# Optimization experiments

Hardware: AMD Instinct MI355X
Metric: run time of the kernel (lower is better)

Reference implementation:

```python
import jax, jax.numpy as jnp
import numpy as np

B, S, D, F, E, SH, K = 2, 2048, 2048, 1024, 16, 2, 2


def setup_inputs() -> dict:
    key = jax.random.key(0)
    ks = jax.random.split(key, 8)
    std = 0.02
    mk = lambda k, sh: (jax.random.normal(k, sh, jnp.float32) * std)
    return {
        "x": jax.random.normal(ks[0], (B, S, D), jnp.float32),
        "wa": mk(ks[1], (D, E)),                      # router, no bias
        "rg": mk(ks[2], (E, D, F)), "rgb": jnp.zeros((E, F), jnp.float32),
        "rw1": mk(ks[3], (E, D, F)), "rb1": jnp.zeros((E, F), jnp.float32),
        "rw2": mk(ks[4], (E, F, D)), "rb2": jnp.zeros((E, D), jnp.float32),
        "sg": mk(ks[5], (SH, D, F)), "sgb": jnp.zeros((SH, F), jnp.float32),
        "sw1": mk(ks[6], (SH, D, F)), "sb1": jnp.zeros((SH, F), jnp.float32),
        "sw2": mk(ks[7], (SH, F, D)), "sb2": jnp.zeros((SH, D), jnp.float32),
    }


def _experts_all(x, g, gb, w1, b1, w2, b2):
    """Run every expert in the stack on every token.
    x: [b,s,d]; g,w1: [e,d,f]; w2: [e,f,d] -> out [b,s,e,d].
    Expert: w2( gelu(gated(x)) * w1(x) ). torch GELU default = exact erf.
    """
    y = jax.nn.gelu(jnp.einsum('bsd,edf->bsef', x, g) + gb, approximate=False)
    y = y * (jnp.einsum('bsd,edf->bsef', x, w1) + b1)
    return jnp.einsum('bsef,efd->bsed', y, w2) + b2


def reference(x, wa, rg, rgb, rw1, rb1, rw2, rb2, sg, sgb, sw1, sb1, sw2, sb2):
    # sigmoid affinity router + top-k, renormalized over the k selected
    aff = jax.nn.sigmoid(jnp.einsum('bsd,de->bse', x, wa))
    topk_p, topk_i = jax.lax.top_k(aff, K)                   # [b,s,k]
    topk_p = topk_p / jnp.sum(topk_p, axis=-1, keepdims=True)
    # dense combine weights [b,s,E]; zero for unselected experts, so the
    # masked-scatter of the original is reproduced exactly by a weighted sum
    combine = jnp.sum(jax.nn.one_hot(topk_i, E, dtype=x.dtype) * topk_p[..., None], axis=2)
    routed = jnp.einsum('bsed,bse->bsd',
                        _experts_all(x, rg, rgb, rw1, rb1, rw2, rb2), combine)
    shared = jnp.sum(_experts_all(x, sg, sgb, sw1, sb1, sw2, sb2), axis=2)
    return x + shared + routed
```

## Files before the change

### kernel.cpp

```cpp
#include <hip/hip_runtime.h>
#include <hip/hip_bf16.h>
#include <math.h>

typedef __bf16 bf16;
typedef bf16  bf16x8 __attribute__((ext_vector_type(8)));
typedef bf16  bf16x4 __attribute__((ext_vector_type(4)));
typedef float f32x4  __attribute__((ext_vector_type(4)));

#define TOKENS 4096
#define DM 2048
#define FF 1024
#define NE 16
#define SH_BASE 12288
#define BK 64

#define WS_CNT    0
#define WS_POS    64
#define WS_BASE   128
#define WS_TOPKW  256
#define WS_TOPKI  33024
#define WS_TSLOT  65792
#define WS_LIST   98560
#define WS_XB     180480
#define WS_H      16957696
#define WS_Y      58900736
#define WS_B1R    142786816
#define WS_B1S    277004544
#define WS_W2TR   293781760
#define WS_W2TS   360890624

__device__ __forceinline__ bf16 f2bf(float f) {
  unsigned u = __builtin_bit_cast(unsigned, f);
  u += 0x7fffu + ((u >> 16) & 1u);
  unsigned short h = (unsigned short)(u >> 16);
  return __builtin_bit_cast(bf16, h);
}

typedef const __attribute__((address_space(1))) void* gas_t;
typedef __attribute__((address_space(3))) void* las_t;
__device__ __forceinline__ void load_lds16(const bf16* g, bf16* l) {
  __builtin_amdgcn_global_load_lds((gas_t)g, (las_t)l, 16, 0, 0);
}

__global__ void cvt_x_kernel(const float* __restrict__ x, bf16* __restrict__ xb) {
  const size_t idx = ((size_t)blockIdx.x * 256 + threadIdx.x) * 4;
  f32x4 v = *(const f32x4*)(x + idx);
  bf16x4 o;
  o[0] = f2bf(v[0]); o[1] = f2bf(v[1]); o[2] = f2bf(v[2]); o[3] = f2bf(v[3]);
  *(bf16x4*)(xb + idx) = o;
}

__global__ void transpose_cvt_kernel(const float* __restrict__ in, bf16* __restrict__ out,
                                     int R, int C) {
  __shared__ float tile[64][65];
  const size_t zo = (size_t)blockIdx.z * R * C;
  const int c0 = blockIdx.x * 64, r0 = blockIdx.y * 64;
  const int t = threadIdx.x;
  const int lr = t >> 2;
  const int lc = (t & 3) * 4;
  const float* src = in + zo + (size_t)(r0 + lr) * C + c0;
#pragma unroll
  for (int j = 0; j < 4; j++) {
    const f32x4 v = *(const f32x4*)(src + lc + j * 16);
    tile[lr][lc + j * 16 + 0] = v[0];
    tile[lr][lc + j * 16 + 1] = v[1];
    tile[lr][lc + j * 16 + 2] = v[2];
    tile[lr][lc + j * 16 + 3] = v[3];
  }
  __syncthreads();
  const int co = t >> 4;
  const int ro = (t & 15) * 4;
#pragma unroll
  for (int j = 0; j < 4; j++) {
    const int c = co + j * 16;
    bf16x4 v;
    v[0] = f2bf(tile[ro + 0][c]);
    v[1] = f2bf(tile[ro + 1][c]);
    v[2] = f2bf(tile[ro + 2][c]);
    v[3] = f2bf(tile[ro + 3][c]);
    *(bf16x4*)(out + zo + (size_t)(c0 + c) * R + r0 + ro) = v;
  }
}

__global__ void transpose_cvt_fused_kernel(const float* __restrict__ in, bf16* __restrict__ out,
                                           int half) {
  __shared__ float tile[64][65];
  const size_t zi = (size_t)blockIdx.z * DM * FF;
  const size_t zo = (size_t)blockIdx.z * (2 * FF) * DM;
  const int c0 = blockIdx.x * 64, r0 = blockIdx.y * 64;
  const int t = threadIdx.x;
  const int lr = t >> 2;
  const int lc = (t & 3) * 4;
  const float* src = in + zi + (size_t)(r0 + lr) * FF + c0;
#pragma unroll
  for (int j = 0; j < 4; j++) {
    const f32x4 v = *(const f32x4*)(src + lc + j * 16);
    tile[lr][lc + j * 16 + 0] = v[0];
    tile[lr][lc + j * 16 + 1] = v[1];
    tile[lr][lc + j * 16 + 2] = v[2];
    tile[lr][lc + j * 16 + 3] = v[3];
  }
  __syncthreads();
  const int co = t >> 4;
  const int ro = (t & 15) * 4;
#pragma unroll
  for (int j = 0; j < 4; j++) {
    const int c = co + j * 16;
    const int f = c0 + c;
    const int fr = ((f >> 4) << 5) + half * 16 + (f & 15);
    bf16x4 v;
    v[0] = f2bf(tile[ro + 0][c]);
    v[1] = f2bf(tile[ro + 1][c]);
    v[2] = f2bf(tile[ro + 2][c]);
    v[3] = f2bf(tile[ro + 3][c]);
    *(bf16x4*)(out + zo + (size_t)fr * DM + r0 + ro) = v;
  }
}

#define RT_TOK 16
#define RT_DK  256
#define RT_PITCH (RT_DK + 4)

__global__ __launch_bounds__(256) void router_kernel(
    const float* __restrict__ x, const float* __restrict__ wa,
    float* __restrict__ topk_w, int* __restrict__ topk_i,
    int* __restrict__ cnt) {
  __shared__ float xs[RT_TOK][RT_PITCH];
  __shared__ float was[NE][RT_PITCH];
  __shared__ float aff[RT_TOK][17];

  const int tid = threadIdx.x;
  const int t = tid >> 4;
  const int e = tid & 15;
  const int t0 = blockIdx.x * RT_TOK;

  f32x4 acc4 = {0.f, 0.f, 0.f, 0.f};

  for (int d0 = 0; d0 < DM; d0 += RT_DK) {
    __syncthreads();
    {
      const int r = tid >> 4;
      const int c4 = (tid & 15) * 4;
      const float* src = x + (size_t)(t0 + r) * DM + d0;
#pragma unroll
      for (int j = 0; j < 4; j++)
        *(f32x4*)(&xs[r][c4 + j * 64]) = *(const f32x4*)(src + c4 + j * 64);
    }
    {
      const int e2 = tid & 15;
      const int dd = (tid >> 4) * 16;
#pragma unroll
      for (int j = 0; j < 16; j++)
        was[e2][dd + j] = wa[(size_t)(d0 + dd + j) * NE + e2];
    }
    __syncthreads();
#pragma unroll 16
    for (int d = 0; d < RT_DK; d += 4) {
      const f32x4 xv = *(const f32x4*)(&xs[t][d]);
      const f32x4 wv = *(const f32x4*)(&was[e][d]);
      acc4 += xv * wv;
    }
  }

  const float a = acc4[0] + acc4[1] + acc4[2] + acc4[3];
  aff[t][e] = 1.f / (1.f + expf(-a));
  __syncthreads();

  if (e == 0) {
    float b0 = -1e30f, b1 = -1e30f; int i0 = 0, i1 = 0;
    for (int i = 0; i < NE; i++) {
      const float v = aff[t][i];
      if (v > b0) { b1 = b0; i1 = i0; b0 = v; i0 = i; }
      else if (v > b1) { b1 = v; i1 = i; }
    }
    const int tok = t0 + t;
    const float inv = 1.f / (b0 + b1);
    topk_w[tok * 2] = b0 * inv;  topk_w[tok * 2 + 1] = b1 * inv;
    topk_i[tok * 2] = i0;        topk_i[tok * 2 + 1] = i1;
    atomicAdd(&cnt[i0], 1);      atomicAdd(&cnt[i1], 1);
  }
}

__global__ void prefix_kernel(const int* __restrict__ cnt, int* __restrict__ base) {
  if (threadIdx.x == 0) {
    int acc = 0;
    for (int e = 0; e < NE; e++) { base[e] = acc; acc += (cnt[e] + 127) & ~127; }
    base[NE] = SH_BASE;
    base[NE + 1] = SH_BASE + TOKENS;
  }
}

__global__ void build_lists_kernel(const int* __restrict__ topk_i, const int* __restrict__ base,
                                   int* __restrict__ pos, int* __restrict__ list,
                                   int* __restrict__ token_slot) {
  const int t = blockIdx.x * 256 + threadIdx.x;
  if (t >= TOKENS) return;
#pragma unroll
  for (int k = 0; k < 2; k++) {
    const int e = topk_i[t * 2 + k];
    const int p = atomicAdd(&pos[e], 1);
    const int slot = base[e] + p;
    list[slot] = t;
    token_slot[t * 2 + k] = slot;
  }
  list[SH_BASE + t] = t;
  list[SH_BASE + TOKENS + t] = t;
}

#define GEMM_GRID_MAX 2304

__device__ __forceinline__ bool map_tile(int flat, const int* __restrict__ cnt,
                                         int& e, int& my, int& nx) {
  int o = 0;
  for (int ee = 0; ee < NE + 2; ++ee) {
    const int ce = (ee < NE) ? cnt[ee] : TOKENS;
    const int me = (ce + 127) >> 7;
    const int Te = me << 4;
    if (flat < o + Te) {
      const int l = flat - o;
      const int s = (l & 7) * (me << 1) + (l >> 3);
      nx = s / me;
      my = s - nx * me;
      e = ee;
      return true;
    }
    o += Te;
  }
  return false;
}

__global__ __launch_bounds__(256, 2) void gemm1_kernel(
    const bf16* __restrict__ xb, const int* __restrict__ list,
    const int* __restrict__ base, const int* __restrict__ cnt,
    const bf16* __restrict__ B1R, const bf16* __restrict__ B1S,
    const float* __restrict__ rgb, const float* __restrict__ rb1,
    const float* __restrict__ sgb, const float* __restrict__ sb1,
    bf16* __restrict__ H) {
  int e, bmy, bnx;
  if (!map_tile(blockIdx.x, cnt, e, bmy, bnx)) return;
  const int ce = (e < NE) ? cnt[e] : TOKENS;
  const int m0 = bmy * 128;
  const int n0 = bnx * 128;
  const int bse = base[e];

  const bf16* B1; const float *gb, *ub;
  if (e < NE) { B1 = B1R + (size_t)e * (2 * FF) * DM; gb = rgb + e * FF; ub = rb1 + e * FF; }
  else { const int s = e - NE; B1 = B1S + (size_t)s * (2 * FF) * DM; gb = sgb + s * FF; ub = sb1 + s * FF; }

  __shared__ bf16 As[2][128 * BK];
  __shared__ bf16 Bs[2][128 * BK];

  const int tid = threadIdx.x, lane = tid & 63, wid = tid >> 6;
  const int lrow = lane >> 3;
  const int laneK = (((lane & 7) ^ lrow) << 3);
  const int q0 = wid << 5;

  const bf16* aP[4];
#pragma unroll
  for (int i = 0; i < 4; i++) {
    int rA = m0 + q0 + (i << 3) + lrow;
    if (rA >= ce) rA = ce - 1;
    aP[i] = xb + (size_t)list[bse + rA] * DM + laneK;
  }
  const bf16* bP = B1 + (size_t)(n0 + q0 + lrow) * DM + laneK;

  const int wm = (wid & 1) * 64, wn = (wid >> 1) * 64;
  const int m16 = lane & 15, quad = lane >> 4, xor7 = m16 & 7;

  f32x4 acc[4][4] = {};

#pragma unroll
  for (int i = 0; i < 4; i++) {
    load_lds16(aP[i], &As[0][(q0 + (i << 3)) * BK + (lane << 3)]);
    load_lds16(bP + (size_t)(i * 8) * DM, &Bs[0][(q0 + (i << 3)) * BK + (lane << 3)]);
  }

  int cur = 0;
  for (int k0 = 0; k0 < DM; k0 += BK) {
    __syncthreads();
    if (k0 + BK < DM) {
      const int nxt = cur ^ 1;
      const int kn = k0 + BK;
#pragma unroll
      for (int i = 0; i < 4; i++) {
        load_lds16(aP[i] + kn, &As[nxt][(q0 + (i << 3)) * BK + (lane << 3)]);
        load_lds16(bP + (size_t)(i * 8) * DM + kn, &Bs[nxt][(q0 + (i << 3)) * BK + (lane << 3)]);
      }
    }
#pragma unroll
    for (int kk = 0; kk < 2; kk++) {
      const int slot = (((kk << 2) + quad) ^ xor7) << 3;
      bf16x8 af[4], bfr[4];
#pragma unroll
      for (int i = 0; i < 4; i++) {
        af[i]  = *(const bf16x8*)(&As[cur][(wm + m16 + 16 * i) * BK + slot]);
        bfr[i] = *(const bf16x8*)(&Bs[cur][(wn + m16 + 16 * i) * BK + slot]);
      }
#pragma unroll
      for (int mi = 0; mi < 4; mi++)
#pragma unroll
        for (int ni = 0; ni < 4; ni++)
          acc[mi][ni] = __builtin_amdgcn_mfma_f32_16x16x32_bf16(af[mi], bfr[ni], acc[mi][ni], 0, 0, 0);
    }
    cur ^= 1;
  }

  const int q4 = quad * 4;
  const int fbase = ((n0 + wn) >> 1) + m16;
#pragma unroll
  for (int mi = 0; mi < 4; mi++) {
#pragma unroll
    for (int nj = 0; nj < 2; nj++) {
      const int f = fbase + nj * 16;
      const float gbv = gb[f], ubv = ub[f];
#pragma unroll
      for (int r = 0; r < 4; r++) {
        const int row = m0 + wm + mi * 16 + q4 + r;
        const float g = acc[mi][2 * nj][r] + gbv;
        const float u = acc[mi][2 * nj + 1][r] + ubv;
        const float h = 0.5f * g * (1.f + erff(g * 0.70710678118f)) * u;
        H[(size_t)(bse + row) * FF + f] = f2bf(h);
      }
    }
  }
}

__global__ __launch_bounds__(256, 2) void gemm2_kernel(
    const bf16* __restrict__ Hb, const int* __restrict__ base, const int* __restrict__ cnt,
    const bf16* __restrict__ rw2T, const bf16* __restrict__ sw2T,
    const float* __restrict__ rb2, const float* __restrict__ sb2,
    bf16* __restrict__ Y) {
  int e, bmy, bnx;
  if (!map_tile(blockIdx.x, cnt, e, bmy, bnx)) return;
  const int m0 = bmy * 128;
  const int n0 = bnx * 128;
  const int bse = base[e];

  const bf16* B; const float* bb;
  if (e < NE) { B = rw2T + (size_t)e * DM * FF; bb = rb2 + e * DM; }
  else { const int s = e - NE; B = sw2T + (size_t)s * DM * FF; bb = sb2 + s * DM; }

  __shared__ bf16 As[2][128 * BK];
  __shared__ bf16 Bs[2][128 * BK];

  const int tid = threadIdx.x, lane = tid & 63, wid = tid >> 6;
  const int lrow = lane >> 3;
  const int laneK = (((lane & 7) ^ lrow) << 3);
  const int q0 = wid << 5;

  const bf16* aP = Hb + (size_t)(bse + m0 + q0 + lrow) * FF + laneK;
  const bf16* bP = B  + (size_t)(n0 + q0 + lrow) * FF + laneK;

  const int wm = (wid & 1) * 64, wn = (wid >> 1) * 64;
  const int m16 = lane & 15, quad = lane >> 4, xor7 = m16 & 7;

  f32x4 acc[4][4] = {};

#pragma unroll
  for (int i = 0; i < 4; i++) {
    load_lds16(aP + (size_t)(i * 8) * FF, &As[0][(q0 + (i << 3)) * BK + (lane << 3)]);
    load_lds16(bP + (size_t)(i * 8) * FF, &Bs[0][(q0 + (i << 3)) * BK + (lane << 3)]);
  }

  int cur = 0;
  for (int k0 = 0; k0 < FF; k0 += BK) {
    __syncthreads();
    if (k0 + BK < FF) {
      const int nxt = cur ^ 1;
      const int kn = k0 + BK;
#pragma unroll
      for (int i = 0; i < 4; i++) {
        load_lds16(aP + (size_t)(i * 8) * FF + kn, &As[nxt][(q0 + (i << 3)) * BK + (lane << 3)]);
        load_lds16(bP + (size_t)(i * 8) * FF + kn, &Bs[nxt][(q0 + (i << 3)) * BK + (lane << 3)]);
      }
    }
#pragma unroll
    for (int kk = 0; kk < 2; kk++) {
      const int slot = (((kk << 2) + quad) ^ xor7) << 3;
      bf16x8 af[4], bfr[4];
#pragma unroll
      for (int i = 0; i < 4; i++) {
        af[i]  = *(const bf16x8*)(&As[cur][(wm + m16 + 16 * i) * BK + slot]);
        bfr[i] = *(const bf16x8*)(&Bs[cur][(wn + m16 + 16 * i) * BK + slot]);
      }
#pragma unroll
      for (int mi = 0; mi < 4; mi++)
#pragma unroll
        for (int ni = 0; ni < 4; ni++)
          acc[mi][ni] = __builtin_amdgcn_mfma_f32_16x16x32_bf16(af[mi], bfr[ni], acc[mi][ni], 0, 0, 0);
    }
    cur ^= 1;
  }

  const int q4 = quad * 4;
#pragma unroll
  for (int mi = 0; mi < 4; mi++) {
#pragma unroll
    for (int ni = 0; ni < 4; ni++) {
      const int n = n0 + wn + ni * 16 + m16;
      const float bv = bb[n];
#pragma unroll
      for (int r = 0; r < 4; r++) {
        const int row = m0 + wm + mi * 16 + q4 + r;
        Y[(size_t)(bse + row) * DM + n] = f2bf(acc[mi][ni][r] + bv);
      }
    }
  }
}

__global__ void combine_kernel(const float* __restrict__ x, const bf16* __restrict__ Y,
                               const int* __restrict__ token_slot, const float* __restrict__ topk_w,
                               float* __restrict__ out) {
  const int t = blockIdx.x;
  const int d = threadIdx.x * 8;
  const int s0 = token_slot[t * 2], s1 = token_slot[t * 2 + 1];
  const float w0 = topk_w[t * 2], w1 = topk_w[t * 2 + 1];
  const bf16x8 ya = *(const bf16x8*)(Y + (size_t)(SH_BASE + t) * DM + d);
  const bf16x8 yb = *(const bf16x8*)(Y + (size_t)(SH_BASE + TOKENS + t) * DM + d);
  const bf16x8 y0 = *(const bf16x8*)(Y + (size_t)s0 * DM + d);
  const bf16x8 y1 = *(const bf16x8*)(Y + (size_t)s1 * DM + d);
  const float* xp = x + (size_t)t * DM + d;
  float* op = out + (size_t)t * DM + d;
#pragma unroll
  for (int j = 0; j < 8; j++)
    op[j] = xp[j] + (float)ya[j] + (float)yb[j] + w0 * (float)y0[j] + w1 * (float)y1[j];
}

extern "C" void kernel_launch(void* const* d_in, const int* in_sizes, int n_in,
                              void* d_out, int out_size, void* d_ws, size_t ws_size,
                              hipStream_t stream) {
  (void)in_sizes; (void)n_in; (void)out_size; (void)ws_size;
  const float* x   = (const float*)d_in[0];
  const float* wa  = (const float*)d_in[1];
  const float* rg  = (const float*)d_in[2];
  const float* rgb = (const float*)d_in[3];
  const float* rw1 = (const float*)d_in[4];
  const float* rb1 = (const float*)d_in[5];
  const float* rw2 = (const float*)d_in[6];
  const float* rb2 = (const float*)d_in[7];
  const float* sg  = (const float*)d_in[8];
  const float* sgb = (const float*)d_in[9];
  const float* sw1 = (const float*)d_in[10];
  const float* sb1 = (const float*)d_in[11];
  const float* sw2 = (const float*)d_in[12];
  const float* sb2 = (const float*)d_in[13];
  float* out = (float*)d_out;

  char* ws = (char*)d_ws;
  int*   cnt        = (int*)(ws + WS_CNT);
  int*   pos        = (int*)(ws + WS_POS);
  int*   basep      = (int*)(ws + WS_BASE);
  float* topk_w     = (float*)(ws + WS_TOPKW);
  int*   topk_i     = (int*)(ws + WS_TOPKI);
  int*   token_slot = (int*)(ws + WS_TSLOT);
  int*   list       = (int*)(ws + WS_LIST);
  bf16*  xb         = (bf16*)(ws + WS_XB);
  bf16*  H          = (bf16*)(ws + WS_H);
  bf16*  Y          = (bf16*)(ws + WS_Y);
  bf16*  B1R        = (bf16*)(ws + WS_B1R);
  bf16*  B1S        = (bf16*)(ws + WS_B1S);
  bf16*  W2TR       = (bf16*)(ws + WS_W2TR);
  bf16*  W2TS       = (bf16*)(ws + WS_W2TS);

  hipMemsetAsync(ws, 0, 128, stream);

  cvt_x_kernel<<<(TOKENS * DM) / 1024, 256, 0, stream>>>(x, xb);
  router_kernel<<<TOKENS / RT_TOK, 256, 0, stream>>>(x, wa, topk_w, topk_i, cnt);
  prefix_kernel<<<1, 64, 0, stream>>>(cnt, basep);
  build_lists_kernel<<<TOKENS / 256, 256, 0, stream>>>(topk_i, basep, pos, list, token_slot);

  transpose_cvt_fused_kernel<<<dim3(FF / 64, DM / 64, NE), 256, 0, stream>>>(rg,  B1R, 0);
  transpose_cvt_fused_kernel<<<dim3(FF / 64, DM / 64, NE), 256, 0, stream>>>(rw1, B1R, 1);
  transpose_cvt_fused_kernel<<<dim3(FF / 64, DM / 64, 2),  256, 0, stream>>>(sg,  B1S, 0);
  transpose_cvt_fused_kernel<<<dim3(FF / 64, DM / 64, 2),  256, 0, stream>>>(sw1, B1S, 1);
  transpose_cvt_kernel<<<dim3(DM / 64, FF / 64, NE), 256, 0, stream>>>(rw2, W2TR, FF, DM);
  transpose_cvt_kernel<<<dim3(DM / 64, FF / 64, 2),  256, 0, stream>>>(sw2, W2TS, FF, DM);

  gemm1_kernel<<<GEMM_GRID_MAX, 256, 0, stream>>>(
      xb, list, basep, cnt, B1R, B1S, rgb, rb1, sgb, sb1, H);
  gemm2_kernel<<<GEMM_GRID_MAX, 256, 0, stream>>>(
      H, basep, cnt, W2TR, W2TS, rb2, sb2, Y);
  combine_kernel<<<TOKENS, 256, 0, stream>>>(x, Y, token_slot, topk_w, out);
}
```

Baseline: 920.8 us.

## Load GEMM A operand directly to registers and merge preprocessing kernels

Both grouped GEMMs stop staging the A operand in LDS and instead read 16-byte fragments straight from global memory into registers, double-buffered alongside the LDS-staged B tile, and occupancy hint rises to 3 blocks per SIMD. The x-to-bf16 conversion is folded into the router kernel, and the six weight transpose launches collapse into two launches. This cuts LDS traffic and footprint plus launch overhead, but A loads become uncoalesced per-lane row reads and register pressure increases.

```diff
diff --git a/kernel.cpp b/kernel.cpp
--- a/kernel.cpp
+++ b/kernel.cpp
@@ -42,23 +42,20 @@
   __builtin_amdgcn_global_load_lds((gas_t)g, (las_t)l, 16, 0, 0);
 }
 
-__global__ void cvt_x_kernel(const float* __restrict__ x, bf16* __restrict__ xb) {
-  const size_t idx = ((size_t)blockIdx.x * 256 + threadIdx.x) * 4;
-  f32x4 v = *(const f32x4*)(x + idx);
-  bf16x4 o;
-  o[0] = f2bf(v[0]); o[1] = f2bf(v[1]); o[2] = f2bf(v[2]); o[3] = f2bf(v[3]);
-  *(bf16x4*)(xb + idx) = o;
-}
-
-__global__ void transpose_cvt_kernel(const float* __restrict__ in, bf16* __restrict__ out,
-                                     int R, int C) {
+__global__ void transpose_cvt_all_kernel(const float* __restrict__ rw2, const float* __restrict__ sw2,
+                                         bf16* __restrict__ W2TR, bf16* __restrict__ W2TS) {
   __shared__ float tile[64][65];
-  const size_t zo = (size_t)blockIdx.z * R * C;
+  const int z = blockIdx.z;
+  const float* src_base;
+  bf16* dst_base;
+  if (z < NE) { src_base = rw2 + (size_t)z * FF * DM; dst_base = W2TR + (size_t)z * DM * FF; }
+  else { const int s = z - NE; src_base = sw2 + (size_t)s * FF * DM; dst_base = W2TS + (size_t)s * DM * FF; }
+  const int R = FF, C = DM;
   const int c0 = blockIdx.x * 64, r0 = blockIdx.y * 64;
   const int t = threadIdx.x;
   const int lr = t >> 2;
   const int lc = (t & 3) * 4;
-  const float* src = in + zo + (size_t)(r0 + lr) * C + c0;
+  const float* src = src_base + (size_t)(r0 + lr) * C + c0;
 #pragma unroll
   for (int j = 0; j < 4; j++) {
     const f32x4 v = *(const f32x4*)(src + lc + j * 16);
@@ -78,20 +75,33 @@
     v[1] = f2bf(tile[ro + 1][c]);
     v[2] = f2bf(tile[ro + 2][c]);
     v[3] = f2bf(tile[ro + 3][c]);
-    *(bf16x4*)(out + zo + (size_t)(c0 + c) * R + r0 + ro) = v;
-  }
-}
-
-__global__ void transpose_cvt_fused_kernel(const float* __restrict__ in, bf16* __restrict__ out,
-                                           int half) {
+    *(bf16x4*)(dst_base + (size_t)(c0 + c) * R + r0 + ro) = v;
+  }
+}
+
+__global__ void transpose_cvt_fused_all_kernel(
+    const float* __restrict__ rg, const float* __restrict__ rw1,
+    const float* __restrict__ sg, const float* __restrict__ sw1,
+    bf16* __restrict__ B1R, bf16* __restrict__ B1S) {
   __shared__ float tile[64][65];
-  const size_t zi = (size_t)blockIdx.z * DM * FF;
-  const size_t zo = (size_t)blockIdx.z * (2 * FF) * DM;
+  const int z = blockIdx.z;
+  const int half = (z >= 18) ? 1 : 0;
+  const int ze = z - 18 * half;
+  const float* src_base;
+  bf16* dst_base;
+  if (ze < NE) {
+    src_base = (half ? rw1 : rg) + (size_t)ze * DM * FF;
+    dst_base = B1R + (size_t)ze * (2 * FF) * DM;
+  } else {
+    const int s = ze - NE;
+    src_base = (half ? sw1 : sg) + (size_t)s * DM * FF;
+    dst_base = B1S + (size_t)s * (2 * FF) * DM;
+  }
   const int c0 = blockIdx.x * 64, r0 = blockIdx.y * 64;
   const int t = threadIdx.x;
   const int lr = t >> 2;
   const int lc = (t & 3) * 4;
-  const float* src = in + zi + (size_t)(r0 + lr) * FF + c0;
+  const float* src = src_base + (size_t)(r0 + lr) * FF + c0;
 #pragma unroll
   for (int j = 0; j < 4; j++) {
     const f32x4 v = *(const f32x4*)(src + lc + j * 16);
@@ -113,7 +123,7 @@
     v[1] = f2bf(tile[ro + 1][c]);
     v[2] = f2bf(tile[ro + 2][c]);
     v[3] = f2bf(tile[ro + 3][c]);
-    *(bf16x4*)(out + zo + (size_t)fr * DM + r0 + ro) = v;
+    *(bf16x4*)(dst_base + (size_t)fr * DM + r0 + ro) = v;
   }
 }
 
@@ -124,7 +134,7 @@
 __global__ __launch_bounds__(256) void router_kernel(
     const float* __restrict__ x, const float* __restrict__ wa,
     float* __restrict__ topk_w, int* __restrict__ topk_i,
-    int* __restrict__ cnt) {
+    int* __restrict__ cnt, bf16* __restrict__ xb) {
   __shared__ float xs[RT_TOK][RT_PITCH];
   __shared__ float was[NE][RT_PITCH];
   __shared__ float aff[RT_TOK][17];
@@ -142,9 +152,15 @@
       const int r = tid >> 4;
       const int c4 = (tid & 15) * 4;
       const float* src = x + (size_t)(t0 + r) * DM + d0;
-#pragma unroll
-      for (int j = 0; j < 4; j++)
-        *(f32x4*)(&xs[r][c4 + j * 64]) = *(const f32x4*)(src + c4 + j * 64);
+      bf16* dstx = xb + (size_t)(t0 + r) * DM + d0;
+#pragma unroll
+      for (int j = 0; j < 4; j++) {
+        const f32x4 v = *(const f32x4*)(src + c4 + j * 64);
+        *(f32x4*)(&xs[r][c4 + j * 64]) = v;
+        bf16x4 o;
+        o[0] = f2bf(v[0]); o[1] = f2bf(v[1]); o[2] = f2bf(v[2]); o[3] = f2bf(v[3]);
+        *(bf16x4*)(dstx + c4 + j * 64) = o;
+      }
     }
     {
       const int e2 = tid & 15;
@@ -229,7 +245,37 @@
   return false;
 }
 
-__global__ __launch_bounds__(256, 2) void gemm1_kernel(
+
+#define LOAD_A(af, kb)                                                      \
+  _Pragma("unroll")                                                         \
+  for (int kk = 0; kk < 2; kk++)                                            \
+    _Pragma("unroll")                                                       \
+    for (int i = 0; i < 4; i++)                                             \
+      af[kk][i] = *(const bf16x8*)(aR[i] + (kb) + kk * 32 + quad * 8);
+
+#define STAGE_B(buf, kof)                                                   \
+  _Pragma("unroll")                                                         \
+  for (int i = 0; i < 4; i++)                                               \
+    load_lds16(bP + (size_t)(i * 8) * LDB + (kof),                          \
+               &Bs[buf][(q0 + (i << 3)) * BK + (lane << 3)]);
+
+#define COMPUTE(af, buf)                                                    \
+  _Pragma("unroll")                                                         \
+  for (int kk = 0; kk < 2; kk++) {                                          \
+    const int slot = (((kk << 2) + quad) ^ xor7) << 3;                      \
+    bf16x8 bfr[4];                                                          \
+    _Pragma("unroll")                                                       \
+    for (int i = 0; i < 4; i++)                                             \
+      bfr[i] = *(const bf16x8*)(&Bs[buf][(wn + m16 + 16 * i) * BK + slot]); \
+    _Pragma("unroll")                                                       \
+    for (int mi = 0; mi < 4; mi++)                                          \
+      _Pragma("unroll")                                                     \
+      for (int ni = 0; ni < 4; ni++)                                        \
+        acc[mi][ni] = __builtin_amdgcn_mfma_f32_16x16x32_bf16(              \
+            af[kk][mi], bfr[ni], acc[mi][ni], 0, 0, 0);                     \
+  }
+
+__global__ __launch_bounds__(256, 3) void gemm1_kernel(
     const bf16* __restrict__ xb, const int* __restrict__ list,
     const int* __restrict__ base, const int* __restrict__ cnt,
     const bf16* __restrict__ B1R, const bf16* __restrict__ B1S,
@@ -247,62 +293,43 @@
   if (e < NE) { B1 = B1R + (size_t)e * (2 * FF) * DM; gb = rgb + e * FF; ub = rb1 + e * FF; }
   else { const int s = e - NE; B1 = B1S + (size_t)s * (2 * FF) * DM; gb = sgb + s * FF; ub = sb1 + s * FF; }
 
-  __shared__ bf16 As[2][128 * BK];
   __shared__ bf16 Bs[2][128 * BK];
 
   const int tid = threadIdx.x, lane = tid & 63, wid = tid >> 6;
   const int lrow = lane >> 3;
   const int laneK = (((lane & 7) ^ lrow) << 3);
   const int q0 = wid << 5;
-
-  const bf16* aP[4];
-#pragma unroll
-  for (int i = 0; i < 4; i++) {
-    int rA = m0 + q0 + (i << 3) + lrow;
-    if (rA >= ce) rA = ce - 1;
-    aP[i] = xb + (size_t)list[bse + rA] * DM + laneK;
-  }
-  const bf16* bP = B1 + (size_t)(n0 + q0 + lrow) * DM + laneK;
-
   const int wm = (wid & 1) * 64, wn = (wid >> 1) * 64;
   const int m16 = lane & 15, quad = lane >> 4, xor7 = m16 & 7;
 
+  const int LDB = DM;
+  const bf16* bP = B1 + (size_t)(n0 + q0 + lrow) * DM + laneK;
+
+  const bf16* aR[4];
+#pragma unroll
+  for (int i = 0; i < 4; i++) {
+    int rA = m0 + wm + m16 + 16 * i;
+    if (rA >= ce) rA = ce - 1;
+    aR[i] = xb + (size_t)list[bse + rA] * DM;
+  }
+
   f32x4 acc[4][4] = {};
-
-#pragma unroll
-  for (int i = 0; i < 4; i++) {
-    load_lds16(aP[i], &As[0][(q0 + (i << 3)) * BK + (lane << 3)]);
-    load_lds16(bP + (size_t)(i * 8) * DM, &Bs[0][(q0 + (i << 3)) * BK + (lane << 3)]);
-  }
-
-  int cur = 0;
-  for (int k0 = 0; k0 < DM; k0 += BK) {
-    __syncthreads();
-    if (k0 + BK < DM) {
-      const int nxt = cur ^ 1;
-      const int kn = k0 + BK;
-#pragma unroll
-      for (int i = 0; i < 4; i++) {
-        load_lds16(aP[i] + kn, &As[nxt][(q0 + (i << 3)) * BK + (lane << 3)]);
-        load_lds16(bP + (size_t)(i * 8) * DM + kn, &Bs[nxt][(q0 + (i << 3)) * BK + (lane << 3)]);
-      }
-    }
-#pragma unroll
-    for (int kk = 0; kk < 2; kk++) {
-      const int slot = (((kk << 2) + quad) ^ xor7) << 3;
-      bf16x8 af[4], bfr[4];
-#pragma unroll
-      for (int i = 0; i < 4; i++) {
-        af[i]  = *(const bf16x8*)(&As[cur][(wm + m16 + 16 * i) * BK + slot]);
-        bfr[i] = *(const bf16x8*)(&Bs[cur][(wn + m16 + 16 * i) * BK + slot]);
-      }
-#pragma unroll
-      for (int mi = 0; mi < 4; mi++)
-#pragma unroll
-        for (int ni = 0; ni < 4; ni++)
-          acc[mi][ni] = __builtin_amdgcn_mfma_f32_16x16x32_bf16(af[mi], bfr[ni], acc[mi][ni], 0, 0, 0);
-    }
-    cur ^= 1;
+  bf16x8 afA[2][4], afB[2][4];
+
+  STAGE_B(0, 0)
+  LOAD_A(afA, 0)
+
+  for (int k0 = 0; k0 < DM; k0 += 2 * BK) {
+    __syncthreads();
+    STAGE_B(1, k0 + BK)
+    LOAD_A(afB, k0 + BK)
+    COMPUTE(afA, 0)
+    __syncthreads();
+    if (k0 + 2 * BK < DM) {
+      STAGE_B(0, k0 + 2 * BK)
+      LOAD_A(afA, k0 + 2 * BK)
+    }
+    COMPUTE(afB, 1)
   }
 
   const int q4 = quad * 4;
@@ -325,7 +352,7 @@
   }
 }
 
-__global__ __launch_bounds__(256, 2) void gemm2_kernel(
+__global__ __launch_bounds__(256, 3) void gemm2_kernel(
     const bf16* __restrict__ Hb, const int* __restrict__ base, const int* __restrict__ cnt,
     const bf16* __restrict__ rw2T, const bf16* __restrict__ sw2T,
     const float* __restrict__ rb2, const float* __restrict__ sb2,
@@ -340,56 +367,40 @@
   if (e < NE) { B = rw2T + (size_t)e * DM * FF; bb = rb2 + e * DM; }
   else { const int s = e - NE; B = sw2T + (size_t)s * DM * FF; bb = sb2 + s * DM; }
 
-  __shared__ bf16 As[2][128 * BK];
   __shared__ bf16 Bs[2][128 * BK];
 
   const int tid = threadIdx.x, lane = tid & 63, wid = tid >> 6;
   const int lrow = lane >> 3;
   const int laneK = (((lane & 7) ^ lrow) << 3);
   const int q0 = wid << 5;
-
-  const bf16* aP = Hb + (size_t)(bse + m0 + q0 + lrow) * FF + laneK;
-  const bf16* bP = B  + (size_t)(n0 + q0 + lrow) * FF + laneK;
-
   const int wm = (wid & 1) * 64, wn = (wid >> 1) * 64;
   const int m16 = lane & 15, quad = lane >> 4, xor7 = m16 & 7;
 
+  const int LDB = FF;
+  const bf16* bP = B + (size_t)(n0 + q0 + lrow) * FF + laneK;
+
+  const bf16* aR[4];
+#pragma unroll
+  for (int i = 0; i < 4; i++)
+    aR[i] = Hb + (size_t)(bse + m0 + wm + m16 + 16 * i) * FF;
+
   f32x4 acc[4][4] = {};
-
-#pragma unroll
-  for (int i = 0; i < 4; i++) {
-    load_lds16(aP + (size_t)(i * 8) * FF, &As[0][(q0 + (i << 3)) * BK + (lane << 3)]);
-    load_lds16(bP + (size_t)(i * 8) * FF, &Bs[0][(q0 + (i << 3)) * BK + (lane << 3)]);
-  }
-
-  int cur = 0;
-  for (int k0 = 0; k0 < FF; k0 += BK) {
-    __syncthreads();
-    if (k0 + BK < FF) {
-      const int nxt = cur ^ 1;
-      const int kn = k0 + BK;
-#pragma unroll
-      for (int i = 0; i < 4; i++) {
-        load_lds16(aP + (size_t)(i * 8) * FF + kn, &As[nxt][(q0 + (i << 3)) * BK + (lane << 3)]);
-        load_lds16(bP + (size_t)(i * 8) * FF + kn, &Bs[nxt][(q0 + (i << 3)) * BK + (lane << 3)]);
-      }
-    }
-#pragma unroll
-    for (int kk = 0; kk < 2; kk++) {
-      const int slot = (((kk << 2) + quad) ^ xor7) << 3;
-      bf16x8 af[4], bfr[4];
-#pragma unroll
-      for (int i = 0; i < 4; i++) {
-        af[i]  = *(const bf16x8*)(&As[cur][(wm + m16 + 16 * i) * BK + slot]);
-        bfr[i] = *(const bf16x8*)(&Bs[cur][(wn + m16 + 16 * i) * BK + slot]);
-      }
-#pragma unroll
-      for (int mi = 0; mi < 4; mi++)
-#pragma unroll
-        for (int ni = 0; ni < 4; ni++)
-          acc[mi][ni] = __builtin_amdgcn_mfma_f32_16x16x32_bf16(af[mi], bfr[ni], acc[mi][ni], 0, 0, 0);
-    }
-    cur ^= 1;
+  bf16x8 afA[2][4], afB[2][4];
+
+  STAGE_B(0, 0)
+  LOAD_A(afA, 0)
+
+  for (int k0 = 0; k0 < FF; k0 += 2 * BK) {
+    __syncthreads();
+    STAGE_B(1, k0 + BK)
+    LOAD_A(afB, k0 + BK)
+    COMPUTE(afA, 0)
+    __syncthreads();
+    if (k0 + 2 * BK < FF) {
+      STAGE_B(0, k0 + 2 * BK)
+      LOAD_A(afA, k0 + 2 * BK)
+    }
+    COMPUTE(afB, 1)
   }
 
   const int q4 = quad * 4;
@@ -459,22 +470,19 @@
   bf16*  Y          = (bf16*)(ws + WS_Y);
   bf16*  B1R        = (bf16*)(ws + WS_B1R);
   bf16*  B1S        = (bf16*)(ws + WS_B1S);
-  bf16*  W2TR       = (bf16*)(ws + WS_W2TR);
-  bf16*  W2TS       = (bf16*)(ws + WS_W2TS);
+  bf16*  W2TR      = (bf16*)(ws + WS_W2TR);
+  bf16*  W2TS      = (bf16*)(ws + WS_W2TS);
 
   hipMemsetAsync(ws, 0, 128, stream);
 
-  cvt_x_kernel<<<(TOKENS * DM) / 1024, 256, 0, stream>>>(x, xb);
-  router_kernel<<<TOKENS / RT_TOK, 256, 0, stream>>>(x, wa, topk_w, topk_i, cnt);
+  router_kernel<<<TOKENS / RT_TOK, 256, 0, stream>>>(x, wa, topk_w, topk_i, cnt, xb);
   prefix_kernel<<<1, 64, 0, stream>>>(cnt, basep);
   build_lists_kernel<<<TOKENS / 256, 256, 0, stream>>>(topk_i, basep, pos, list, token_slot);
 
-  transpose_cvt_fused_kernel<<<dim3(FF / 64, DM / 64, NE), 256, 0, stream>>>(rg,  B1R, 0);
-  transpose_cvt_fused_kernel<<<dim3(FF / 64, DM / 64, NE), 256, 0, stream>>>(rw1, B1R, 1);
-  transpose_cvt_fused_kernel<<<dim3(FF / 64, DM / 64, 2),  256, 0, stream>>>(sg,  B1S, 0);
-  transpose_cvt_fused_kernel<<<dim3(FF / 64, DM / 64, 2),  256, 0, stream>>>(sw1, B1S, 1);
-  transpose_cvt_kernel<<<dim3(DM / 64, FF / 64, NE), 256, 0, stream>>>(rw2, W2TR, FF, DM);
-  transpose_cvt_kernel<<<dim3(DM / 64, FF / 64, 2),  256, 0, stream>>>(sw2, W2TS, FF, DM);
+  transpose_cvt_fused_all_kernel<<<dim3(FF / 64, DM / 64, 36), 256, 0, stream>>>(
+      rg, rw1, sg, sw1, B1R, B1S);
+  transpose_cvt_all_kernel<<<dim3(DM / 64, FF / 64, 18), 256, 0, stream>>>(
+      rw2, sw2, W2TR, W2TS);
 
   gemm1_kernel<<<GEMM_GRID_MAX, 256, 0, stream>>>(
       xb, list, basep, cnt, B1R, B1S, rgb, rb1, sgb, sb1, H);
```

Result: slower. 1.088 ms (+18.2%).
